# Kernel tuning notes

Measured on AMD Instinct MI355X. Metric: run time of the kernel, lower is better.

## Reference

```python
import jax, jax.numpy as jnp
import numpy as np

NUM_HEADS = 12
D_T, D_H, D_W = 192, 288, 288  # rope_dims for embed_dim=768


def rotate_half(x):
    x1, x2 = jnp.split(x, 2, axis=-1)
    return jnp.concatenate([-x2, x1], axis=-1)


def apply_rope(qk, cos_t, sin_t, cos_h, sin_h, cos_w, sin_w, t_idx, h_idx, w_idx):
    # qk: (B, N, C); rotate the three dim-chunks with per-token gathered tables
    qk_t = qk[..., :D_T]
    qk_h = qk[..., D_T:D_T + D_H]
    qk_w = qk[..., D_T + D_H:]
    qk_t = qk_t * cos_t[t_idx] + rotate_half(qk_t) * sin_t[t_idx]
    qk_h = qk_h * cos_h[h_idx] + rotate_half(qk_h) * sin_h[h_idx]
    qk_w = qk_w * cos_w[w_idx] + rotate_half(qk_w) * sin_w[w_idx]
    return jnp.concatenate([qk_t, qk_h, qk_w], axis=-1)


def setup_inputs() -> dict:
    key = jax.random.key(0)
    ks = jax.random.split(key, 12)
    B, N, C = 2, 2048, 768
    T, Hs, Ws = 8, 16, 16  # N = T*Hs*Ws
    x = jax.random.normal(ks[0], (B, N, C), dtype=jnp.float32)
    Wqkv = jax.random.normal(ks[1], (C, 3 * C), dtype=jnp.float32) * (C ** -0.5)
    Wout = jax.random.normal(ks[2], (C, C), dtype=jnp.float32) * (C ** -0.5)
    cos_t = jax.random.uniform(ks[3], (T, D_T), dtype=jnp.float32)
    sin_t = jax.random.uniform(ks[4], (T, D_T), dtype=jnp.float32)
    cos_h = jax.random.uniform(ks[5], (Hs, D_H), dtype=jnp.float32)
    sin_h = jax.random.uniform(ks[6], (Hs, D_H), dtype=jnp.float32)
    cos_w = jax.random.uniform(ks[7], (Ws, D_W), dtype=jnp.float32)
    sin_w = jax.random.uniform(ks[8], (Ws, D_W), dtype=jnp.float32)
    t_idx = jax.random.randint(ks[9], (N,), 0, T, dtype=jnp.int32)
    h_idx = jax.random.randint(ks[10], (N,), 0, Hs, dtype=jnp.int32)
    w_idx = jax.random.randint(ks[11], (N,), 0, Ws, dtype=jnp.int32)
    return {"x": x, "Wqkv": Wqkv, "Wout": Wout,
            "cos_t": cos_t, "sin_t": sin_t, "cos_h": cos_h, "sin_h": sin_h,
            "cos_w": cos_w, "sin_w": sin_w,
            "t_idx": t_idx, "h_idx": h_idx, "w_idx": w_idx}


def reference(x, Wqkv, Wout, cos_t, sin_t, cos_h, sin_h, cos_w, sin_w, t_idx, h_idx, w_idx):
    B, N, C = x.shape
    Hd = C // NUM_HEADS
    scale = Hd ** -0.5
    qkv = (x @ Wqkv).reshape(B, N, 3, C)
    q, k, v = qkv[:, :, 0], qkv[:, :, 1], qkv[:, :, 2]
    # RoPE applied to full embedding dim BEFORE head split
    q = apply_rope(q, cos_t, sin_t, cos_h, sin_h, cos_w, sin_w, t_idx, h_idx, w_idx)
    k = apply_rope(k, cos_t, sin_t, cos_h, sin_h, cos_w, sin_w, t_idx, h_idx, w_idx)
    q = q.reshape(B, N, NUM_HEADS, Hd).transpose(0, 2, 1, 3)
    k = k.reshape(B, N, NUM_HEADS, Hd).transpose(0, 2, 1, 3)
    v = v.reshape(B, N, NUM_HEADS, Hd).transpose(0, 2, 1, 3)
    attn = jnp.einsum('bhqd,bhkd->bhqk', q, k) * scale
    attn = jax.nn.softmax(attn, axis=-1)
    out = jnp.einsum('bhqk,bhkd->bhqd', attn, v)
    out = out.transpose(0, 2, 1, 3).reshape(B, N, C)
    return out @ Wout
```

## Files before the change

### kernel.cpp

```cpp
#include <hip/hip_runtime.h>
#include <hip/hip_bf16.h>
#include <math.h>

#define BB 2
#define NN 2048
#define CC 768
#define NHEAD 12
#define HD 64
#define C3 2304

typedef __attribute__((ext_vector_type(8))) _Float16 half8;
typedef __attribute__((ext_vector_type(8))) short short8;
typedef __attribute__((ext_vector_type(4))) float f32x4;
typedef __attribute__((ext_vector_type(4))) unsigned uint4v;
#define MFMAH(a, b, c) \
  __builtin_amdgcn_mfma_f32_16x16x32_f16(a, b, c, 0, 0, 0)

__device__ __forceinline__ float fast_exp2(float x) {
  return __builtin_amdgcn_exp2f(x);
}
__device__ __forceinline__ ushort f2h(float x) {
  _Float16 h = (_Float16)x;
  return __builtin_bit_cast(ushort, h);
}
__device__ __forceinline__ unsigned pk2h(float a, float b) {
  return __builtin_bit_cast(unsigned, __builtin_amdgcn_cvt_pkrtz(a, b));
}
__device__ __forceinline__ void gload_lds16(const void* gsrc, void* lds) {
  __builtin_amdgcn_global_load_lds(
      (const __attribute__((address_space(1))) unsigned int*)gsrc,
      (__attribute__((address_space(3))) unsigned int*)lds, 16, 0, 0);
}
__device__ __forceinline__ half8 ld_h8(const ushort* p) {
  return __builtin_bit_cast(half8, *reinterpret_cast<const short8*>(p));
}

__global__ __launch_bounds__(256) void conv_rows_kernel(const float* __restrict__ X,
                                                        ushort* __restrict__ Xf) {
  int idx = blockIdx.x * 256 + threadIdx.x;
  const float4 v0 = *reinterpret_cast<const float4*>(&X[(size_t)idx * 8]);
  const float4 v1 = *reinterpret_cast<const float4*>(&X[(size_t)idx * 8 + 4]);
  ushort h[8] = {f2h(v0.x), f2h(v0.y), f2h(v0.z), f2h(v0.w),
                 f2h(v1.x), f2h(v1.y), f2h(v1.z), f2h(v1.w)};
  *reinterpret_cast<uint4*>(&Xf[(size_t)idx * 8]) = *reinterpret_cast<uint4*>(h);
}

__global__ __launch_bounds__(256) void conv_transpose_kernel(const float* __restrict__ W,
                                                             ushort* __restrict__ Wf,
                                                             int N) {
  __shared__ float t[32][33];
  const int tx = threadIdx.x & 31, ty = threadIdx.x >> 5;
  const int n0 = blockIdx.x * 32, k0 = blockIdx.y * 32;
#pragma unroll
  for (int r = 0; r < 4; r++) {
    int kk = ty + r * 8;
    t[kk][tx] = W[(size_t)(k0 + kk) * N + n0 + tx];
  }
  __syncthreads();
#pragma unroll
  for (int r = 0; r < 4; r++) {
    int nn = ty + r * 8;
    Wf[(size_t)(n0 + nn) * CC + k0 + tx] = f2h(t[tx][nn]);
  }
}

template <int BM>
__global__ __launch_bounds__(256) void gemm_f16_kernel(const ushort* __restrict__ A,
                                                       const ushort* __restrict__ B,
                                                       float* __restrict__ C, int Nn) {
  constexpr int WM = BM / 2;
  constexpr int MR = WM / 16;
  constexpr int NR = 3;
  __shared__ __align__(16) ushort Asm[BM * 64];
  __shared__ __align__(16) ushort Bsm[96 * 64];
  const int tid = threadIdx.x;
  const int lane = tid & 63, w = tid >> 6;
  const int l15 = lane & 15, lg = lane >> 4;
  const int wr = w >> 1, wc = w & 1;
  const int m0 = blockIdx.y * BM, n0 = blockIdx.x * 96;
  const int srow = lane >> 3, lc = lane & 7;
  const int scp = lc ^ (srow & 7);

  f32x4 acc[MR][NR];
#pragma unroll
  for (int m = 0; m < MR; m++)
#pragma unroll
    for (int n = 0; n < NR; n++) acc[m][n] = (f32x4){0.f, 0.f, 0.f, 0.f};

  for (int k0 = 0; k0 < 768; k0 += 64) {
#pragma unroll
    for (int it = 0; it < BM / 32; it++) {
      int r0 = it * 32 + w * 8;
      int row = r0 + srow;
      gload_lds16(A + (size_t)(m0 + row) * CC + k0 + scp * 8, &Asm[r0 * 64]);
    }
#pragma unroll
    for (int it = 0; it < 3; it++) {
      int r0 = it * 32 + w * 8;
      int row = r0 + srow;
      gload_lds16(B + (size_t)(n0 + row) * CC + k0 + scp * 8, &Bsm[r0 * 64]);
    }
    __syncthreads();

    half8 ah[MR][2], bh[NR][2];
#pragma unroll
    for (int m = 0; m < MR; m++) {
      int row = wr * WM + m * 16 + l15;
#pragma unroll
      for (int s = 0; s < 2; s++)
        ah[m][s] = ld_h8(&Asm[row * 64 + ((s * 4 + lg) ^ (row & 7)) * 8]);
    }
#pragma unroll
    for (int n = 0; n < NR; n++) {
      int col = wc * 48 + n * 16 + l15;
#pragma unroll
      for (int s = 0; s < 2; s++)
        bh[n][s] = ld_h8(&Bsm[col * 64 + ((s * 4 + lg) ^ (col & 7)) * 8]);
    }
#pragma unroll
    for (int s = 0; s < 2; s++)
#pragma unroll
      for (int m = 0; m < MR; m++)
#pragma unroll
        for (int n = 0; n < NR; n++)
          acc[m][n] = MFMAH(ah[m][s], bh[n][s], acc[m][n]);
    __syncthreads();
  }

#pragma unroll
  for (int m = 0; m < MR; m++)
#pragma unroll
    for (int j = 0; j < 4; j++) {
      int row = m0 + wr * WM + m * 16 + lg * 4 + j;
#pragma unroll
      for (int n = 0; n < NR; n++)
        C[(size_t)row * Nn + n0 + wc * 48 + n * 16 + l15] = acc[m][n][j];
    }
}

__global__ __launch_bounds__(256) void rope_f16_kernel(
    const float* __restrict__ qkv, const float* __restrict__ cos_t,
    const float* __restrict__ sin_t, const float* __restrict__ cos_h,
    const float* __restrict__ sin_h, const float* __restrict__ cos_w,
    const float* __restrict__ sin_w, const int* __restrict__ t_idx,
    const int* __restrict__ h_idx, const int* __restrict__ w_idx,
    ushort* __restrict__ Qf, ushort* __restrict__ Kf) {
  const int tok = blockIdx.x;
  const int b = tok >> 11, n = tok & 2047;
  const int ti = t_idx[n], hi = h_idx[n], wi = w_idx[n];
  const float* base = qkv + (size_t)tok * C3;
  const float QSC = 0.125f * 1.44269504088896f;

#pragma unroll
  for (int s = 0; s < 3; s++) {
    int j = threadIdx.x + s * 256;
    float c, sn, sign;
    int pj;
    if (j < 192) {
      int jj = j;
      c = cos_t[ti * 192 + jj];
      sn = sin_t[ti * 192 + jj];
      pj = (jj < 96) ? j + 96 : j - 96;
      sign = (jj < 96) ? -1.f : 1.f;
    } else if (j < 480) {
      int jj = j - 192;
      c = cos_h[hi * 288 + jj];
      sn = sin_h[hi * 288 + jj];
      pj = (jj < 144) ? j + 144 : j - 144;
      sign = (jj < 144) ? -1.f : 1.f;
    } else {
      int jj = j - 480;
      c = cos_w[wi * 288 + jj];
      sn = sin_w[wi * 288 + jj];
      pj = (jj < 144) ? j + 144 : j - 144;
      sign = (jj < 144) ? -1.f : 1.f;
    }
    float qv = base[j], kv = base[768 + j];
    float qp = base[pj] * sign, kp = base[768 + pj] * sign;
    float qr = fmaf(qv, c, qp * sn) * QSC;
    float kr = fmaf(kv, c, kp * sn);
    int h = j >> 6, d = j & 63;
    int bh = b * NHEAD + h;
    size_t o = ((size_t)bh * NN + n) * HD + d;
    Qf[o] = f2h(qr);
    Kf[o] = f2h(kr);
  }
}

__global__ __launch_bounds__(256) void v_transpose_kernel(const float* __restrict__ qkv,
                                                          ushort* __restrict__ Vt) {
  __shared__ ushort t[64][70];
  const int bh = blockIdx.y;
  const int n0 = blockIdx.x * 64;
  const int b = bh / NHEAD, h = bh % NHEAD;
  const int row = threadIdx.x >> 2;
  const int c0 = (threadIdx.x & 3) * 16;
  const float* src = qkv + (size_t)(b * NN + n0 + row) * C3 + 1536 + h * 64 + c0;
#pragma unroll
  for (int i = 0; i < 16; i += 4) {
    float4 v = *reinterpret_cast<const float4*>(src + i);
    t[row][c0 + i + 0] = f2h(v.x);
    t[row][c0 + i + 1] = f2h(v.y);
    t[row][c0 + i + 2] = f2h(v.z);
    t[row][c0 + i + 3] = f2h(v.w);
  }
  __syncthreads();
  const int d = threadIdx.x >> 2;
  const int tk0 = (threadIdx.x & 3) * 16;
  ushort tmp[16];
#pragma unroll
  for (int i = 0; i < 16; i++) tmp[i] = t[tk0 + i][d];
  ushort* dst = Vt + ((size_t)bh * HD + d) * NN + n0 + tk0;
  *reinterpret_cast<uint4*>(dst) = *reinterpret_cast<uint4*>(tmp);
  *reinterpret_cast<uint4*>(dst + 8) = *reinterpret_cast<uint4*>(tmp + 8);
}

__global__ __launch_bounds__(256, 3) void attn_mfma_kernel(
    const ushort* __restrict__ Qf, const ushort* __restrict__ Kf,
    const ushort* __restrict__ Vt, float* __restrict__ PartO,
    float* __restrict__ Partml) {
  __shared__ __align__(16) ushort smem[2][2][4096];
  const int tid = threadIdx.x;
  const int lane = tid & 63, w = tid >> 6;
  const int l15 = lane & 15, lg = lane >> 4;
  const int qt = blockIdx.x;
  const int bh = blockIdx.y;
  const int sp = blockIdx.z;
  const size_t kbase = (size_t)bh * NN * HD;
  const size_t vbase = (size_t)bh * HD * NN;

  half8 qf[2][2];
#pragma unroll
  for (int qs = 0; qs < 2; qs++) {
    const int r = qt * 128 + qs * 64 + w * 16 + l15;
#pragma unroll
    for (int s = 0; s < 2; s++)
      qf[qs][s] = ld_h8(Qf + kbase + (size_t)r * HD + s * 32 + lg * 8);
  }

  const int srow = lane >> 3;
  const int sc = (lane & 7) ^ srow;

#define STAGE(kt_, bb_)                                                        \
  {                                                                            \
    _Pragma("unroll") for (int it = 0; it < 2; it++) {                         \
      int r0 = it * 32 + w * 8;                                                \
      int r = r0 + srow;                                                       \
      gload_lds16(Kf + kbase + (size_t)((kt_)*64 + r) * 64 + sc * 8,           \
                  &smem[bb_][0][r0 * 64]);                                     \
      gload_lds16(Vt + vbase + (size_t)r * NN + (kt_)*64 + sc * 8,             \
                  &smem[bb_][1][r0 * 64]);                                     \
    }                                                                          \
  }

  f32x4 o_acc[2][4];
#pragma unroll
  for (int qs = 0; qs < 2; qs++)
#pragma unroll
    for (int g = 0; g < 4; g++) o_acc[qs][g] = (f32x4){0.f, 0.f, 0.f, 0.f};
  float m_run[2] = {-INFINITY, -INFINITY};
  float l_run[2] = {0.f, 0.f};

  const int rmask7 = l15 & 7;
  const int gsel0 = (lg < 2) ? 0 : 1;
  const bool send_own = ((lg ^ (lg >> 1)) & 1) != 0;
  const int kt0 = sp * 16, ktend = sp * 16 + 16;

  STAGE(kt0, 0);

  for (int kt = kt0; kt < ktend; kt++) {
    const int cur = (kt - kt0) & 1;
    __syncthreads();
    if (kt + 1 < ktend) STAGE(kt + 1, cur ^ 1);

    const ushort* KB = smem[cur][0];
    const ushort* VB = smem[cur][1];

    f32x4 s_acc[2][4];
#pragma unroll
    for (int qs = 0; qs < 2; qs++)
#pragma unroll
      for (int g = 0; g < 4; g++) s_acc[qs][g] = (f32x4){0.f, 0.f, 0.f, 0.f};
    __builtin_amdgcn_s_setprio(1);
#pragma unroll
    for (int g = 0; g < 4; g++) {
      const int r = g * 16 + l15;
#pragma unroll
      for (int s = 0; s < 2; s++) {
        half8 ka = ld_h8(&KB[r * 64 + ((s * 4 + lg) ^ rmask7) * 8]);
#pragma unroll
        for (int qs = 0; qs < 2; qs++)
          s_acc[qs][g] = MFMAH(ka, qf[qs][s], s_acc[qs][g]);
      }
    }
    __builtin_amdgcn_s_setprio(0);

    half8 pb[2][2];
#pragma unroll
    for (int qs = 0; qs < 2; qs++) {
      float pm = -INFINITY;
#pragma unroll
      for (int g = 0; g < 4; g++)
#pragma unroll
        for (int j = 0; j < 4; j++) pm = fmaxf(pm, s_acc[qs][g][j]);
      pm = fmaxf(pm, __shfl_xor(pm, 16, 64));
      pm = fmaxf(pm, __shfl_xor(pm, 32, 64));
      if (!__all(pm - m_run[qs] <= 8.0f)) {
        const float mn = fmaxf(m_run[qs], pm);
        const float corr = fast_exp2(m_run[qs] - mn);
        m_run[qs] = mn;
        l_run[qs] *= corr;
#pragma unroll
        for (int g = 0; g < 4; g++)
#pragma unroll
          for (int j = 0; j < 4; j++) o_acc[qs][g][j] *= corr;
      }
      float p[4][4];
#pragma unroll
      for (int g = 0; g < 4; g++)
#pragma unroll
        for (int j = 0; j < 4; j++) {
          p[g][j] = fast_exp2(s_acc[qs][g][j] - m_run[qs]);
          l_run[qs] += p[g][j];
        }

      unsigned w0[4], w1[4];
#pragma unroll
      for (int g = 0; g < 4; g++) {
        w0[g] = pk2h(p[g][0], p[g][1]);
        w1[g] = pk2h(p[g][2], p[g][3]);
      }
      const int c0 = gsel0 ^ 1, c1 = c0 + 2;
      unsigned o0 = w0[gsel0], o1 = w1[gsel0], o2 = w0[gsel0 + 2], o3 = w1[gsel0 + 2];
      unsigned r0v = __shfl_xor((int)w0[c0], 32, 64);
      unsigned r1v = __shfl_xor((int)w1[c0], 32, 64);
      unsigned r2v = __shfl_xor((int)w0[c1], 32, 64);
      unsigned r3v = __shfl_xor((int)w1[c1], 32, 64);
      unsigned p0 = send_own ? o0 : r0v, p1 = send_own ? o1 : r1v;
      unsigned p2 = send_own ? o2 : r2v, p3 = send_own ? o3 : r3v;
      unsigned k0v = send_own ? r0v : o0, k1v = send_own ? r1v : o1;
      unsigned k2v = send_own ? r2v : o2, k3v = send_own ? r3v : o3;
      unsigned n0 = __shfl_xor((int)p0, 16, 64);
      unsigned n1 = __shfl_xor((int)p1, 16, 64);
      unsigned n2 = __shfl_xor((int)p2, 16, 64);
      unsigned n3 = __shfl_xor((int)p3, 16, 64);
      const bool lgeven = (lg & 1) == 0;
      uint4v bv0 = lgeven ? (uint4v){k0v, k1v, n0, n1} : (uint4v){n0, n1, k0v, k1v};
      uint4v bv1 = lgeven ? (uint4v){k2v, k3v, n2, n3} : (uint4v){n2, n3, k2v, k3v};
      pb[qs][0] = __builtin_bit_cast(half8, bv0);
      pb[qs][1] = __builtin_bit_cast(half8, bv1);
    }

    __builtin_amdgcn_s_setprio(1);
#pragma unroll
    for (int kk = 0; kk < 2; kk++)
#pragma unroll
      for (int g = 0; g < 4; g++) {
        half8 va = ld_h8(&VB[(g * 16 + l15) * 64 + ((kk * 4 + lg) ^ rmask7) * 8]);
#pragma unroll
        for (int qs = 0; qs < 2; qs++)
          o_acc[qs][g] = MFMAH(va, pb[qs][kk], o_acc[qs][g]);
      }
    __builtin_amdgcn_s_setprio(0);
  }

#pragma unroll
  for (int qs = 0; qs < 2; qs++) {
    float lr = l_run[qs];
    lr += __shfl_xor(lr, 16, 64);
    lr += __shfl_xor(lr, 32, 64);
    const int q = qt * 128 + qs * 64 + w * 16 + l15;
    const size_t pidx = ((size_t)(sp * 24 + bh) * NN + q);
#pragma unroll
    for (int g = 0; g < 4; g++) {
      *reinterpret_cast<float4*>(&PartO[pidx * 64 + g * 16 + lg * 4]) =
          make_float4(o_acc[qs][g][0], o_acc[qs][g][1], o_acc[qs][g][2], o_acc[qs][g][3]);
    }
    if (lg == 0) {
      Partml[pidx * 2] = m_run[qs];
      Partml[pidx * 2 + 1] = lr;
    }
  }
#undef STAGE
}

__global__ __launch_bounds__(256) void attn_combine_kernel(
    const float* __restrict__ PartO, const float* __restrict__ Partml,
    ushort* __restrict__ Attnf) {
  const int qt = blockIdx.x;
  const int bh = blockIdx.y;
  const int b = bh / NHEAD, h = bh % NHEAD;
  const int tid = threadIdx.x;
  const int q = qt * 64 + (tid >> 2);
  const int d0 = (tid & 3) * 16;
  const size_t i0 = ((size_t)bh * NN + q);
  const size_t i1 = ((size_t)(24 + bh) * NN + q);
  const float m0 = Partml[i0 * 2], l0 = Partml[i0 * 2 + 1];
  const float m1 = Partml[i1 * 2], l1 = Partml[i1 * 2 + 1];
  const float m = fmaxf(m0, m1);
  const float w0 = fast_exp2(m0 - m), w1 = fast_exp2(m1 - m);
  const float inv = 1.0f / (l0 * w0 + l1 * w1);

  ushort hv[16];
#pragma unroll
  for (int d = 0; d < 16; d += 4) {
    float4 a = *reinterpret_cast<const float4*>(&PartO[i0 * 64 + d0 + d]);
    float4 bvv = *reinterpret_cast<const float4*>(&PartO[i1 * 64 + d0 + d]);
    hv[d + 0] = f2h((a.x * w0 + bvv.x * w1) * inv);
    hv[d + 1] = f2h((a.y * w0 + bvv.y * w1) * inv);
    hv[d + 2] = f2h((a.z * w0 + bvv.z * w1) * inv);
    hv[d + 3] = f2h((a.w * w0 + bvv.w * w1) * inv);
  }
  ushort* dst = Attnf + (size_t)(b * NN + q) * CC + h * 64 + d0;
  *reinterpret_cast<uint4*>(dst) = *reinterpret_cast<uint4*>(hv);
  *reinterpret_cast<uint4*>(dst + 8) = *reinterpret_cast<uint4*>(hv + 8);
}

extern "C" void kernel_launch(void* const* d_in, const int* in_sizes, int n_in,
                              void* d_out, int out_size, void* d_ws, size_t ws_size,
                              hipStream_t stream) {
  const float* x = (const float*)d_in[0];
  const float* Wqkv = (const float*)d_in[1];
  const float* Wout = (const float*)d_in[2];
  const float* cos_t = (const float*)d_in[3];
  const float* sin_t = (const float*)d_in[4];
  const float* cos_h = (const float*)d_in[5];
  const float* sin_h = (const float*)d_in[6];
  const float* cos_w = (const float*)d_in[7];
  const float* sin_w = (const float*)d_in[8];
  const int* t_idx = (const int*)d_in[9];
  const int* h_idx = (const int*)d_in[10];
  const int* w_idx = (const int*)d_in[11];
  float* out = (float*)d_out;

  float* ws = (float*)d_ws;
  float* qkv = ws;
  float* PartO = qkv;
  ushort* us = (ushort*)(qkv + (size_t)4096 * 2304);
  const size_t HS = (size_t)24 * 2048 * 64;
  ushort* Qf = us;
  ushort* Kf = Qf + HS;
  ushort* Vt = Kf + HS;
  ushort* xf = Vt + HS;
  ushort* wqf = xf + (size_t)4096 * 768;
  ushort* wof = wqf + (size_t)2304 * 768;
  ushort* attnf = wof + (size_t)768 * 768;
  float* Partml = (float*)(attnf + (size_t)4096 * 768);

  conv_rows_kernel<<<dim3(4096 * 768 / 8 / 256), 256, 0, stream>>>(x, xf);
  conv_transpose_kernel<<<dim3(C3 / 32, CC / 32), 256, 0, stream>>>(Wqkv, wqf, C3);
  conv_transpose_kernel<<<dim3(CC / 32, CC / 32), 256, 0, stream>>>(Wout, wof, CC);
  gemm_f16_kernel<128><<<dim3(C3 / 96, 4096 / 128), 256, 0, stream>>>(xf, wqf, qkv, C3);
  rope_f16_kernel<<<dim3(BB * NN), 256, 0, stream>>>(qkv, cos_t, sin_t, cos_h, sin_h,
                                                     cos_w, sin_w, t_idx, h_idx, w_idx,
                                                     Qf, Kf);
  v_transpose_kernel<<<dim3(NN / 64, BB * NHEAD), 256, 0, stream>>>(qkv, Vt);
  attn_mfma_kernel<<<dim3(NN / 128, BB * NHEAD, 2), 256, 0, stream>>>(Qf, Kf, Vt, PartO,
                                                                      Partml);
  attn_combine_kernel<<<dim3(NN / 64, BB * NHEAD), 256, 0, stream>>>(PartO, Partml,
                                                                     attnf);
  gemm_f16_kernel<64><<<dim3(CC / 96, 4096 / 64), 256, 0, stream>>>(attnf, wof, out, CC);
}
```

Baseline: 121.6 us.

## Split attention KV into four chunks, single-buffer K, raise occupancy target

Raises the attention split-KV factor from two to four, so the grid quadruples in the KV dimension and each block handles eight KV tiles. K staging drops to a single LDS buffer refilled after the QK MFMAs behind an extra barrier, while V stays double-buffered. This cuts LDS per block so launch bounds can request six blocks per CU. The combine kernel is generalised to merge NSP partials, and the workspace layout changes so PartO has its own region. The cost is more partial-output traffic, a larger combine step, an extra sync per tile, and more register pressure under the higher occupancy target.

New measurement: 246.1 us. 102% more time.

```diff
diff --git a/kernel.cpp b/kernel.cpp
--- a/kernel.cpp
+++ b/kernel.cpp
@@ -8,6 +8,7 @@
 #define NHEAD 12
 #define HD 64
 #define C3 2304
+#define NSP 4
 
 typedef __attribute__((ext_vector_type(8))) _Float16 half8;
 typedef __attribute__((ext_vector_type(8))) short short8;
@@ -215,11 +216,12 @@
   *reinterpret_cast<uint4*>(dst + 8) = *reinterpret_cast<uint4*>(tmp + 8);
 }
 
-__global__ __launch_bounds__(256, 3) void attn_mfma_kernel(
+__global__ __launch_bounds__(256, 6) void attn_mfma_kernel(
     const ushort* __restrict__ Qf, const ushort* __restrict__ Kf,
     const ushort* __restrict__ Vt, float* __restrict__ PartO,
     float* __restrict__ Partml) {
-  __shared__ __align__(16) ushort smem[2][2][4096];
+  __shared__ __align__(16) ushort smemK[4096];
+  __shared__ __align__(16) ushort smemV[2][4096];
   const int tid = threadIdx.x;
   const int lane = tid & 63, w = tid >> 6;
   const int l15 = lane & 15, lg = lane >> 4;
@@ -241,15 +243,22 @@
   const int srow = lane >> 3;
   const int sc = (lane & 7) ^ srow;
 
-#define STAGE(kt_, bb_)                                                        \
+#define STAGE_K(kt_)                                                           \
   {                                                                            \
     _Pragma("unroll") for (int it = 0; it < 2; it++) {                         \
       int r0 = it * 32 + w * 8;                                                \
       int r = r0 + srow;                                                       \
       gload_lds16(Kf + kbase + (size_t)((kt_)*64 + r) * 64 + sc * 8,           \
-                  &smem[bb_][0][r0 * 64]);                                     \
+                  &smemK[r0 * 64]);                                            \
+    }                                                                          \
+  }
+#define STAGE_V(kt_, vb_)                                                      \
+  {                                                                            \
+    _Pragma("unroll") for (int it = 0; it < 2; it++) {                         \
+      int r0 = it * 32 + w * 8;                                                \
+      int r = r0 + srow;                                                       \
       gload_lds16(Vt + vbase + (size_t)r * NN + (kt_)*64 + sc * 8,             \
-                  &smem[bb_][1][r0 * 64]);                                     \
+                  &smemV[vb_][r0 * 64]);                                       \
     }                                                                          \
   }
 
@@ -264,17 +273,15 @@
   const int rmask7 = l15 & 7;
   const int gsel0 = (lg < 2) ? 0 : 1;
   const bool send_own = ((lg ^ (lg >> 1)) & 1) != 0;
-  const int kt0 = sp * 16, ktend = sp * 16 + 16;
-
-  STAGE(kt0, 0);
+  const int kt0 = sp * (32 / NSP), ktend = kt0 + (32 / NSP);
+
+  STAGE_V(kt0, 0);
+  STAGE_K(kt0);
 
   for (int kt = kt0; kt < ktend; kt++) {
     const int cur = (kt - kt0) & 1;
     __syncthreads();
-    if (kt + 1 < ktend) STAGE(kt + 1, cur ^ 1);
-
-    const ushort* KB = smem[cur][0];
-    const ushort* VB = smem[cur][1];
+    if (kt + 1 < ktend) STAGE_V(kt + 1, cur ^ 1);
 
     f32x4 s_acc[2][4];
 #pragma unroll
@@ -287,7 +294,7 @@
       const int r = g * 16 + l15;
 #pragma unroll
       for (int s = 0; s < 2; s++) {
-        half8 ka = ld_h8(&KB[r * 64 + ((s * 4 + lg) ^ rmask7) * 8]);
+        half8 ka = ld_h8(&smemK[r * 64 + ((s * 4 + lg) ^ rmask7) * 8]);
 #pragma unroll
         for (int qs = 0; qs < 2; qs++)
           s_acc[qs][g] = MFMAH(ka, qf[qs][s], s_acc[qs][g]);
@@ -295,14 +302,21 @@
     }
     __builtin_amdgcn_s_setprio(0);
 
+    __syncthreads();
+    if (kt + 1 < ktend) STAGE_K(kt + 1);
+
     half8 pb[2][2];
 #pragma unroll
     for (int qs = 0; qs < 2; qs++) {
-      float pm = -INFINITY;
-#pragma unroll
-      for (int g = 0; g < 4; g++)
-#pragma unroll
-        for (int j = 0; j < 4; j++) pm = fmaxf(pm, s_acc[qs][g][j]);
+      float m0a = fmaxf(fmaxf(s_acc[qs][0][0], s_acc[qs][0][1]),
+                        fmaxf(s_acc[qs][0][2], s_acc[qs][0][3]));
+      float m1a = fmaxf(fmaxf(s_acc[qs][1][0], s_acc[qs][1][1]),
+                        fmaxf(s_acc[qs][1][2], s_acc[qs][1][3]));
+      float m2a = fmaxf(fmaxf(s_acc[qs][2][0], s_acc[qs][2][1]),
+                        fmaxf(s_acc[qs][2][2], s_acc[qs][2][3]));
+      float m3a = fmaxf(fmaxf(s_acc[qs][3][0], s_acc[qs][3][1]),
+                        fmaxf(s_acc[qs][3][2], s_acc[qs][3][3]));
+      float pm = fmaxf(fmaxf(m0a, m1a), fmaxf(m2a, m3a));
       pm = fmaxf(pm, __shfl_xor(pm, 16, 64));
       pm = fmaxf(pm, __shfl_xor(pm, 32, 64));
       if (!__all(pm - m_run[qs] <= 8.0f)) {
@@ -356,7 +370,8 @@
     for (int kk = 0; kk < 2; kk++)
 #pragma unroll
       for (int g = 0; g < 4; g++) {
-        half8 va = ld_h8(&VB[(g * 16 + l15) * 64 + ((kk * 4 + lg) ^ rmask7) * 8]);
+        half8 va =
+            ld_h8(&smemV[cur][(g * 16 + l15) * 64 + ((kk * 4 + lg) ^ rmask7) * 8]);
 #pragma unroll
         for (int qs = 0; qs < 2; qs++)
           o_acc[qs][g] = MFMAH(va, pb[qs][kk], o_acc[qs][g]);
@@ -381,7 +396,8 @@
       Partml[pidx * 2 + 1] = lr;
     }
   }
-#undef STAGE
+#undef STAGE_K
+#undef STAGE_V
 }
 
 __global__ __launch_bounds__(256) void attn_combine_kernel(
@@ -393,23 +409,39 @@
   const int tid = threadIdx.x;
   const int q = qt * 64 + (tid >> 2);
   const int d0 = (tid & 3) * 16;
-  const size_t i0 = ((size_t)bh * NN + q);
-  const size_t i1 = ((size_t)(24 + bh) * NN + q);
-  const float m0 = Partml[i0 * 2], l0 = Partml[i0 * 2 + 1];
-  const float m1 = Partml[i1 * 2], l1 = Partml[i1 * 2 + 1];
-  const float m = fmaxf(m0, m1);
-  const float w0 = fast_exp2(m0 - m), w1 = fast_exp2(m1 - m);
-  const float inv = 1.0f / (l0 * w0 + l1 * w1);
+
+  size_t idx[NSP];
+  float mv[NSP], lv[NSP];
+  float m = -INFINITY;
+#pragma unroll
+  for (int s = 0; s < NSP; s++) {
+    idx[s] = ((size_t)(s * 24 + bh) * NN + q);
+    mv[s] = Partml[idx[s] * 2];
+    lv[s] = Partml[idx[s] * 2 + 1];
+    m = fmaxf(m, mv[s]);
+  }
+  float wsum = 0.f, wgt[NSP];
+#pragma unroll
+  for (int s = 0; s < NSP; s++) {
+    wgt[s] = fast_exp2(mv[s] - m);
+    wsum += lv[s] * wgt[s];
+  }
+  const float inv = 1.0f / wsum;
 
   ushort hv[16];
 #pragma unroll
   for (int d = 0; d < 16; d += 4) {
-    float4 a = *reinterpret_cast<const float4*>(&PartO[i0 * 64 + d0 + d]);
-    float4 bvv = *reinterpret_cast<const float4*>(&PartO[i1 * 64 + d0 + d]);
-    hv[d + 0] = f2h((a.x * w0 + bvv.x * w1) * inv);
-    hv[d + 1] = f2h((a.y * w0 + bvv.y * w1) * inv);
-    hv[d + 2] = f2h((a.z * w0 + bvv.z * w1) * inv);
-    hv[d + 3] = f2h((a.w * w0 + bvv.w * w1) * inv);
+    float acc[4] = {0.f, 0.f, 0.f, 0.f};
+#pragma unroll
+    for (int s = 0; s < NSP; s++) {
+      float4 a = *reinterpret_cast<const float4*>(&PartO[idx[s] * 64 + d0 + d]);
+      acc[0] = fmaf(a.x, wgt[s], acc[0]);
+      acc[1] = fmaf(a.y, wgt[s], acc[1]);
+      acc[2] = fmaf(a.z, wgt[s], acc[2]);
+      acc[3] = fmaf(a.w, wgt[s], acc[3]);
+    }
+#pragma unroll
+    for (int i = 0; i < 4; i++) hv[d + i] = f2h(acc[i] * inv);
   }
   ushort* dst = Attnf + (size_t)(b * NN + q) * CC + h * 64 + d0;
   *reinterpret_cast<uint4*>(dst) = *reinterpret_cast<uint4*>(hv);
@@ -433,10 +465,11 @@
   const int* w_idx = (const int*)d_in[11];
   float* out = (float*)d_out;
 
+  const size_t R0 = (size_t)NSP * 24 * 2048 * 64;
   float* ws = (float*)d_ws;
   float* qkv = ws;
-  float* PartO = qkv;
-  ushort* us = (ushort*)(qkv + (size_t)4096 * 2304);
+  float* PartO = ws;
+  ushort* us = (ushort*)(ws + R0);
   const size_t HS = (size_t)24 * 2048 * 64;
   ushort* Qf = us;
   ushort* Kf = Qf + HS;
@@ -455,8 +488,8 @@
                                                      cos_w, sin_w, t_idx, h_idx, w_idx,
                                                      Qf, Kf);
   v_transpose_kernel<<<dim3(NN / 64, BB * NHEAD), 256, 0, stream>>>(qkv, Vt);
-  attn_mfma_kernel<<<dim3(NN / 128, BB * NHEAD, 2), 256, 0, stream>>>(Qf, Kf, Vt, PartO,
-                                                                      Partml);
+  attn_mfma_kernel<<<dim3(NN / 128, BB * NHEAD, NSP), 256, 0, stream>>>(Qf, Kf, Vt,
+                                                                        PartO, Partml);
   attn_combine_kernel<<<dim3(NN / 64, BB * NHEAD), 256, 0, stream>>>(PartO, Partml,
                                                                      attnf);
   gemm_f16_kernel<64><<<dim3(CC / 96, 4096 / 64), 256, 0, stream>>>(attnf, wof, out, CC);
```

## Emit fp16 QKV from GEMM and drop split-KV attention with combine pass

Applied to the files above, without the earlier changes.

The QKV GEMM now writes fp16 instead of fp32, which halves its store traffic and the reads in the RoPE and V-transpose kernels. The attention kernel no longer splits the key range in two. Each block walks all keys, normalizes and writes fp16 output directly, so the combine kernel and the partial O/m/l buffers are removed. The trade-off is half as many attention blocks (384), which lowers parallelism on a large GPU, and a small precision loss from rounding the QKV intermediate to fp16. The row-max reduction is also rewritten as a tree.

After: 129.7 us. +6.6%, slower.

```diff
diff --git a/kernel.cpp b/kernel.cpp
--- a/kernel.cpp
+++ b/kernel.cpp
@@ -22,6 +22,9 @@
 __device__ __forceinline__ ushort f2h(float x) {
   _Float16 h = (_Float16)x;
   return __builtin_bit_cast(ushort, h);
+}
+__device__ __forceinline__ float h2f(ushort u) {
+  return (float)__builtin_bit_cast(_Float16, u);
 }
 __device__ __forceinline__ unsigned pk2h(float a, float b) {
   return __builtin_bit_cast(unsigned, __builtin_amdgcn_cvt_pkrtz(a, b));
@@ -64,10 +67,10 @@
   }
 }
 
-template <int BM>
+template <int BM, bool F16OUT>
 __global__ __launch_bounds__(256) void gemm_f16_kernel(const ushort* __restrict__ A,
                                                        const ushort* __restrict__ B,
-                                                       float* __restrict__ C, int Nn) {
+                                                       void* __restrict__ Cout, int Nn) {
   constexpr int WM = BM / 2;
   constexpr int MR = WM / 16;
   constexpr int NR = 3;
@@ -133,13 +136,19 @@
     for (int j = 0; j < 4; j++) {
       int row = m0 + wr * WM + m * 16 + lg * 4 + j;
 #pragma unroll
-      for (int n = 0; n < NR; n++)
-        C[(size_t)row * Nn + n0 + wc * 48 + n * 16 + l15] = acc[m][n][j];
+      for (int n = 0; n < NR; n++) {
+        int col = n0 + wc * 48 + n * 16 + l15;
+        if constexpr (F16OUT) {
+          ((ushort*)Cout)[(size_t)row * Nn + col] = f2h(acc[m][n][j]);
+        } else {
+          ((float*)Cout)[(size_t)row * Nn + col] = acc[m][n][j];
+        }
+      }
     }
 }
 
 __global__ __launch_bounds__(256) void rope_f16_kernel(
-    const float* __restrict__ qkv, const float* __restrict__ cos_t,
+    const ushort* __restrict__ qkvh, const float* __restrict__ cos_t,
     const float* __restrict__ sin_t, const float* __restrict__ cos_h,
     const float* __restrict__ sin_h, const float* __restrict__ cos_w,
     const float* __restrict__ sin_w, const int* __restrict__ t_idx,
@@ -148,7 +157,7 @@
   const int tok = blockIdx.x;
   const int b = tok >> 11, n = tok & 2047;
   const int ti = t_idx[n], hi = h_idx[n], wi = w_idx[n];
-  const float* base = qkv + (size_t)tok * C3;
+  const ushort* base = qkvh + (size_t)tok * C3;
   const float QSC = 0.125f * 1.44269504088896f;
 
 #pragma unroll
@@ -175,8 +184,8 @@
       pj = (jj < 144) ? j + 144 : j - 144;
       sign = (jj < 144) ? -1.f : 1.f;
     }
-    float qv = base[j], kv = base[768 + j];
-    float qp = base[pj] * sign, kp = base[768 + pj] * sign;
+    float qv = h2f(base[j]), kv = h2f(base[768 + j]);
+    float qp = h2f(base[pj]) * sign, kp = h2f(base[768 + pj]) * sign;
     float qr = fmaf(qv, c, qp * sn) * QSC;
     float kr = fmaf(kv, c, kp * sn);
     int h = j >> 6, d = j & 63;
@@ -187,7 +196,7 @@
   }
 }
 
-__global__ __launch_bounds__(256) void v_transpose_kernel(const float* __restrict__ qkv,
+__global__ __launch_bounds__(256) void v_transpose_kernel(const ushort* __restrict__ qkvh,
                                                           ushort* __restrict__ Vt) {
   __shared__ ushort t[64][70];
   const int bh = blockIdx.y;
@@ -195,15 +204,12 @@
   const int b = bh / NHEAD, h = bh % NHEAD;
   const int row = threadIdx.x >> 2;
   const int c0 = (threadIdx.x & 3) * 16;
-  const float* src = qkv + (size_t)(b * NN + n0 + row) * C3 + 1536 + h * 64 + c0;
-#pragma unroll
-  for (int i = 0; i < 16; i += 4) {
-    float4 v = *reinterpret_cast<const float4*>(src + i);
-    t[row][c0 + i + 0] = f2h(v.x);
-    t[row][c0 + i + 1] = f2h(v.y);
-    t[row][c0 + i + 2] = f2h(v.z);
-    t[row][c0 + i + 3] = f2h(v.w);
-  }
+  const ushort* src = qkvh + (size_t)(b * NN + n0 + row) * C3 + 1536 + h * 64 + c0;
+  ushort tmp16[16];
+  *reinterpret_cast<uint4*>(tmp16) = *reinterpret_cast<const uint4*>(src);
+  *reinterpret_cast<uint4*>(tmp16 + 8) = *reinterpret_cast<const uint4*>(src + 8);
+#pragma unroll
+  for (int i = 0; i < 16; i++) t[row][c0 + i] = tmp16[i];
   __syncthreads();
   const int d = threadIdx.x >> 2;
   const int tk0 = (threadIdx.x & 3) * 16;
@@ -217,15 +223,14 @@
 
 __global__ __launch_bounds__(256, 3) void attn_mfma_kernel(
     const ushort* __restrict__ Qf, const ushort* __restrict__ Kf,
-    const ushort* __restrict__ Vt, float* __restrict__ PartO,
-    float* __restrict__ Partml) {
+    const ushort* __restrict__ Vt, ushort* __restrict__ Attnf) {
   __shared__ __align__(16) ushort smem[2][2][4096];
   const int tid = threadIdx.x;
   const int lane = tid & 63, w = tid >> 6;
   const int l15 = lane & 15, lg = lane >> 4;
   const int qt = blockIdx.x;
   const int bh = blockIdx.y;
-  const int sp = blockIdx.z;
+  const int b = bh / NHEAD, h = bh % NHEAD;
   const size_t kbase = (size_t)bh * NN * HD;
   const size_t vbase = (size_t)bh * HD * NN;
 
@@ -264,14 +269,13 @@
   const int rmask7 = l15 & 7;
   const int gsel0 = (lg < 2) ? 0 : 1;
   const bool send_own = ((lg ^ (lg >> 1)) & 1) != 0;
-  const int kt0 = sp * 16, ktend = sp * 16 + 16;
-
-  STAGE(kt0, 0);
-
-  for (int kt = kt0; kt < ktend; kt++) {
-    const int cur = (kt - kt0) & 1;
+
+  STAGE(0, 0);
+
+  for (int kt = 0; kt < NN / 64; kt++) {
+    const int cur = kt & 1;
     __syncthreads();
-    if (kt + 1 < ktend) STAGE(kt + 1, cur ^ 1);
+    if (kt + 1 < NN / 64) STAGE(kt + 1, cur ^ 1);
 
     const ushort* KB = smem[cur][0];
     const ushort* VB = smem[cur][1];
@@ -298,11 +302,15 @@
     half8 pb[2][2];
 #pragma unroll
     for (int qs = 0; qs < 2; qs++) {
-      float pm = -INFINITY;
-#pragma unroll
-      for (int g = 0; g < 4; g++)
-#pragma unroll
-        for (int j = 0; j < 4; j++) pm = fmaxf(pm, s_acc[qs][g][j]);
+      float m0a = fmaxf(fmaxf(s_acc[qs][0][0], s_acc[qs][0][1]),
+                        fmaxf(s_acc[qs][0][2], s_acc[qs][0][3]));
+      float m1a = fmaxf(fmaxf(s_acc[qs][1][0], s_acc[qs][1][1]),
+                        fmaxf(s_acc[qs][1][2], s_acc[qs][1][3]));
+      float m2a = fmaxf(fmaxf(s_acc[qs][2][0], s_acc[qs][2][1]),
+                        fmaxf(s_acc[qs][2][2], s_acc[qs][2][3]));
+      float m3a = fmaxf(fmaxf(s_acc[qs][3][0], s_acc[qs][3][1]),
+                        fmaxf(s_acc[qs][3][2], s_acc[qs][3][3]));
+      float pm = fmaxf(fmaxf(m0a, m1a), fmaxf(m2a, m3a));
       pm = fmaxf(pm, __shfl_xor(pm, 16, 64));
       pm = fmaxf(pm, __shfl_xor(pm, 32, 64));
       if (!__all(pm - m_run[qs] <= 8.0f)) {
@@ -369,51 +377,17 @@
     float lr = l_run[qs];
     lr += __shfl_xor(lr, 16, 64);
     lr += __shfl_xor(lr, 32, 64);
+    const float inv = 1.0f / lr;
     const int q = qt * 128 + qs * 64 + w * 16 + l15;
-    const size_t pidx = ((size_t)(sp * 24 + bh) * NN + q);
+    ushort* dst = Attnf + (size_t)(b * NN + q) * CC + h * 64;
 #pragma unroll
     for (int g = 0; g < 4; g++) {
-      *reinterpret_cast<float4*>(&PartO[pidx * 64 + g * 16 + lg * 4]) =
-          make_float4(o_acc[qs][g][0], o_acc[qs][g][1], o_acc[qs][g][2], o_acc[qs][g][3]);
-    }
-    if (lg == 0) {
-      Partml[pidx * 2] = m_run[qs];
-      Partml[pidx * 2 + 1] = lr;
+      unsigned lo = pk2h(o_acc[qs][g][0] * inv, o_acc[qs][g][1] * inv);
+      unsigned hi = pk2h(o_acc[qs][g][2] * inv, o_acc[qs][g][3] * inv);
+      *reinterpret_cast<uint2*>(dst + g * 16 + lg * 4) = make_uint2(lo, hi);
     }
   }
 #undef STAGE
-}
-
-__global__ __launch_bounds__(256) void attn_combine_kernel(
-    const float* __restrict__ PartO, const float* __restrict__ Partml,
-    ushort* __restrict__ Attnf) {
-  const int qt = blockIdx.x;
-  const int bh = blockIdx.y;
-  const int b = bh / NHEAD, h = bh % NHEAD;
-  const int tid = threadIdx.x;
-  const int q = qt * 64 + (tid >> 2);
-  const int d0 = (tid & 3) * 16;
-  const size_t i0 = ((size_t)bh * NN + q);
-  const size_t i1 = ((size_t)(24 + bh) * NN + q);
-  const float m0 = Partml[i0 * 2], l0 = Partml[i0 * 2 + 1];
-  const float m1 = Partml[i1 * 2], l1 = Partml[i1 * 2 + 1];
-  const float m = fmaxf(m0, m1);
-  const float w0 = fast_exp2(m0 - m), w1 = fast_exp2(m1 - m);
-  const float inv = 1.0f / (l0 * w0 + l1 * w1);
-
-  ushort hv[16];
-#pragma unroll
-  for (int d = 0; d < 16; d += 4) {
-    float4 a = *reinterpret_cast<const float4*>(&PartO[i0 * 64 + d0 + d]);
-    float4 bvv = *reinterpret_cast<const float4*>(&PartO[i1 * 64 + d0 + d]);
-    hv[d + 0] = f2h((a.x * w0 + bvv.x * w1) * inv);
-    hv[d + 1] = f2h((a.y * w0 + bvv.y * w1) * inv);
-    hv[d + 2] = f2h((a.z * w0 + bvv.z * w1) * inv);
-    hv[d + 3] = f2h((a.w * w0 + bvv.w * w1) * inv);
-  }
-  ushort* dst = Attnf + (size_t)(b * NN + q) * CC + h * 64 + d0;
-  *reinterpret_cast<uint4*>(dst) = *reinterpret_cast<uint4*>(hv);
-  *reinterpret_cast<uint4*>(dst + 8) = *reinterpret_cast<uint4*>(hv + 8);
 }
 
 extern "C" void kernel_launch(void* const* d_in, const int* in_sizes, int n_in,
@@ -434,9 +408,8 @@
   float* out = (float*)d_out;
 
   float* ws = (float*)d_ws;
-  float* qkv = ws;
-  float* PartO = qkv;
-  ushort* us = (ushort*)(qkv + (size_t)4096 * 2304);
+  ushort* qkvh = (ushort*)ws;
+  ushort* us = (ushort*)(ws + (size_t)4096 * 2304 / 2);
   const size_t HS = (size_t)24 * 2048 * 64;
   ushort* Qf = us;
   ushort* Kf = Qf + HS;
@@ -445,19 +418,17 @@
   ushort* wqf = xf + (size_t)4096 * 768;
   ushort* wof = wqf + (size_t)2304 * 768;
   ushort* attnf = wof + (size_t)768 * 768;
-  float* Partml = (float*)(attnf + (size_t)4096 * 768);
 
   conv_rows_kernel<<<dim3(4096 * 768 / 8 / 256), 256, 0, stream>>>(x, xf);
   conv_transpose_kernel<<<dim3(C3 / 32, CC / 32), 256, 0, stream>>>(Wqkv, wqf, C3);
   conv_transpose_kernel<<<dim3(CC / 32, CC / 32), 256, 0, stream>>>(Wout, wof, CC);
-  gemm_f16_kernel<128><<<dim3(C3 / 96, 4096 / 128), 256, 0, stream>>>(xf, wqf, qkv, C3);
-  rope_f16_kernel<<<dim3(BB * NN), 256, 0, stream>>>(qkv, cos_t, sin_t, cos_h, sin_h,
+  gemm_f16_kernel<128, true><<<dim3(C3 / 96, 4096 / 128), 256, 0, stream>>>(xf, wqf,
+                                                                            qkvh, C3);
+  rope_f16_kernel<<<dim3(BB * NN), 256, 0, stream>>>(qkvh, cos_t, sin_t, cos_h, sin_h,
                                                      cos_w, sin_w, t_idx, h_idx, w_idx,
                                                      Qf, Kf);
-  v_transpose_kernel<<<dim3(NN / 64, BB * NHEAD), 256, 0, stream>>>(qkv, Vt);
-  attn_mfma_kernel<<<dim3(NN / 128, BB * NHEAD, 2), 256, 0, stream>>>(Qf, Kf, Vt, PartO,
-                                                                      Partml);
-  attn_combine_kernel<<<dim3(NN / 64, BB * NHEAD), 256, 0, stream>>>(PartO, Partml,
-                                                                     attnf);
-  gemm_f16_kernel<64><<<dim3(CC / 96, 4096 / 64), 256, 0, stream>>>(attnf, wof, out, CC);
-}
+  v_transpose_kernel<<<dim3(NN / 64, BB * NHEAD), 256, 0, stream>>>(qkvh, Vt);
+  attn_mfma_kernel<<<dim3(NN / 128, BB * NHEAD), 256, 0, stream>>>(Qf, Kf, Vt, attnf);
+  gemm_f16_kernel<64, false><<<dim3(CC / 96, 4096 / 64), 256, 0, stream>>>(attnf, wof,
+                                                                           out, CC);
+}
```
